# Performance work log

Hardware: AMD Instinct MI355X
Metric: run time of the kernel (lower is better)

The kernel has to match this reference:

```python
import jax, jax.numpy as jnp
import numpy as np

NUM_CLASSES = 80
STRIDES = (32, 16, 8)
SCORE_THRESH = 0.01
NMS_THRESH = 0.45
TOP_K = 200
PRE_K = 4096          # pre-NMS candidate cap (greedy NMS only ever emits TOP_K boxes)
NEG = -1e9            # 'suppressed' score sentinel (avoids -inf NaN issues)
CLS_OFFSET = 4096.0   # class-aware NMS: offset boxes per class (boxes live in [0, 608])

_ANCHORS_PX = [[(116, 90), (156, 198), (373, 326)],
               [(30, 61), (62, 45), (59, 119)],
               [(10, 13), (16, 30), (33, 23)]]


def setup_inputs() -> dict:
    key = jax.random.key(0)
    bs, img = 8, 608
    inp = {}
    for lvl, (stride, anc) in enumerate(zip(STRIDES, _ANCHORS_PX)):
        H = W = img // stride
        key, k = jax.random.split(key)
        inp[f"in{lvl}"] = jax.random.normal(k, (bs, 3 * (NUM_CLASSES + 5), H, W), dtype=jnp.float32)
        aw = jnp.array([a[0] / stride for a in anc], jnp.float32)
        ah = jnp.array([a[1] / stride for a in anc], jnp.float32)
        inp[f"aw{lvl}"] = jnp.broadcast_to(aw[None, :, None, None], (bs, 3, H, W))
        inp[f"ah{lvl}"] = jnp.broadcast_to(ah[None, :, None, None], (bs, 3, H, W))
        inp[f"gx{lvl}"] = jnp.broadcast_to(jnp.arange(W, dtype=jnp.float32)[None, None, None, :], (bs, 3, H, W))
        inp[f"gy{lvl}"] = jnp.broadcast_to(jnp.arange(H, dtype=jnp.float32)[None, None, :, None], (bs, 3, H, W))
    return inp


def _decode_level(x, aw, ah, gx, gy, stride):
    bs, _, H, W = x.shape
    x = x.reshape(bs, -1, NUM_CLASSES + 5, H, W).transpose(0, 1, 3, 4, 2)  # [bs,3,H,W,85]
    px = jax.nn.sigmoid(x[..., 0]) + gx
    py = jax.nn.sigmoid(x[..., 1]) + gy
    pw = jnp.exp(x[..., 2]) * aw
    ph = jnp.exp(x[..., 3]) * ah
    conf = jax.nn.sigmoid(x[..., 4])
    cls = jax.nn.sigmoid(x[..., 5:])
    boxes = jnp.stack([px, py, pw, ph], -1) * jnp.float32(stride)  # [bs,3,H,W,4] (cx,cy,w,h)
    return boxes.reshape(bs, -1, 4), conf.reshape(bs, -1), cls.reshape(bs, -1, NUM_CLASSES)


def _center_to_corner(b):
    cx, cy, w, h = b[..., 0], b[..., 1], b[..., 2], b[..., 3]
    return jnp.stack([cx - w / 2, cy - h / 2, cx + w / 2, cy + h / 2], -1)


def _nms_image(boxes, conf, cls):
    # boxes [N,4] corner, conf [N], cls [N,C]
    N, C = cls.shape
    scores = (conf[:, None] * cls).reshape(-1)                          # [N*C]
    cboxes = jnp.broadcast_to(boxes[:, None, :], (N, C, 4)).reshape(-1, 4)
    labels = jnp.broadcast_to(jnp.arange(C), (N, C)).reshape(-1)
    s = jnp.where(scores > SCORE_THRESH, scores, NEG)
    top_s, idx = jax.lax.top_k(s, PRE_K)
    b = cboxes[idx]                                                     # [PRE_K,4]
    l = labels[idx]
    ob = b + (l.astype(jnp.float32) * CLS_OFFSET)[:, None]              # class-aware offset
    area = (ob[:, 2] - ob[:, 0]) * (ob[:, 3] - ob[:, 1])

    def step(live, _):
        i = jnp.argmax(live)
        si, bi, ai = live[i], ob[i], area[i]
        x1 = jnp.maximum(bi[0], ob[:, 0]); y1 = jnp.maximum(bi[1], ob[:, 1])
        x2 = jnp.minimum(bi[2], ob[:, 2]); y2 = jnp.minimum(bi[3], ob[:, 3])
        inter = jnp.clip(x2 - x1, 0.0) * jnp.clip(y2 - y1, 0.0)
        iou = inter / (ai + area - inter + 1e-9)
        live = jnp.where(iou > NMS_THRESH, NEG, live)                   # suppresses self too
        return live, (i, si)

    _, (sel, sel_s) = jax.lax.scan(step, top_s, None, length=TOP_K)
    valid = sel_s > SCORE_THRESH
    out_b = jnp.where(valid[:, None], b[sel], 0.0)
    out_l = jnp.where(valid, l[sel], 0).astype(jnp.float32)
    out_s = jnp.where(valid, sel_s, 0.0)
    return jnp.concatenate([out_b, out_l[:, None], out_s[:, None]], -1)  # [TOP_K, 6]


def _forward(levels):
    boxes, conf, cls = [], [], []
    for (x, aw, ah, gx, gy), stride in zip(levels, STRIDES):
        bb, cc, cl = _decode_level(x, aw, ah, gx, gy, stride)
        boxes.append(bb); conf.append(cc); cls.append(cl)
    boxes = _center_to_corner(jnp.concatenate(boxes, 1))   # [bs,N,4]
    conf = jnp.concatenate(conf, 1)                        # [bs,N]
    cls = jnp.concatenate(cls, 1)                          # [bs,N,C]
    return jax.vmap(_nms_image)(boxes, conf, cls)          # [bs,TOP_K,6]


def reference(in0, aw0, ah0, gx0, gy0, in1, aw1, ah1, gx1, gy1, in2, aw2, ah2, gx2, gy2):
    levels = [(in0, aw0, ah0, gx0, gy0), (in1, aw1, ah1, gx1, gy1), (in2, aw2, ah2, gx2, gy2)]
    return _forward(levels)
```

## Files before the change

### kernel.cpp

```cpp
#include <hip/hip_runtime.h>
#include <stdint.h>

typedef unsigned int u32;
typedef unsigned long long u64;

#define NCLS 80
#define NBOX 22743
#define PREK 4096
#define BCAP 65536
#define NIMG 8
#define SCORE_TH 0.01f
#define IOU_TH 0.45f
#define TOPK 200

#define DCH 20
#define DNCH 4
#define GCH 10
#define GNCH 8

#define LCAP 1536

#define BKCAP 8
#define HCAP 224
#define HUGE_TH 3488.0f

#define RJC 4
#define RJW 1024

#define CBINS 512
#define CBIN_BASE 7680u

#define HIST_OFF 0
#define CNT_OFF  16384
#define ZERO_BYTES 18432
#define WIN_OFF  18432
#define BND_OFF  280576
#define PART_OFF BND_OFF
#define BOX_OFF  4474880
#define SKEY_OFF 7385984
#define SOBOX_OFF 7648128
#define SAREA_OFF 8172416

__device__ __forceinline__ float sigmf(float x) { return 1.0f / (1.0f + expf(-x)); }

__device__ __forceinline__ u64 pad_key(int i) { return (u64)(~(u32)i); }

__global__ __launch_bounds__(256) void init_k(uint4* __restrict__ ws) {
  const int i = blockIdx.x * 256 + threadIdx.x;
  if (i < ZERO_BYTES / 16) ws[i] = make_uint4(0u, 0u, 0u, 0u);
}

__global__ __launch_bounds__(256) void decode_hist_all(const float* __restrict__ in0,
                              const float* __restrict__ in1, const float* __restrict__ in2,
                              float4* __restrict__ boxes, u32* __restrict__ hist) {
  __shared__ u32 lh[CBINS];
  const int img = blockIdx.y;
  const int c0 = blockIdx.z * DCH;
  for (int i = threadIdx.x; i < CBINS; i += 256) lh[i] = 0;
  __syncthreads();

  const int bx = blockIdx.x;
  if (bx < 5) {
    const int W = 19, HW = 361;
    const int r = bx * 256 + threadIdx.x;
    if (r < 3 * HW) {
      const int a = r / HW, p = r - a * HW;
      const int y = p / W, x = p - y * W;
      const float* base = in0 + ((size_t)(img * 255 + a * 85)) * (size_t)HW + p;
      float l[DCH];
#pragma unroll
      for (int k = 0; k < DCH; ++k) l[k] = base[(size_t)(5 + c0 + k) * HW];
      const float x4 = base[4 * (size_t)HW];
      if (c0 == 0) {
        const float aw = (a == 0) ? 3.625f : ((a == 1) ? 4.875f : 11.65625f);
        const float ah = (a == 0) ? 2.8125f : ((a == 1) ? 6.1875f : 10.1875f);
        const float x0 = base[0];
        const float x1 = base[(size_t)HW];
        const float x2 = base[2 * (size_t)HW];
        const float x3 = base[3 * (size_t)HW];
        const float px = sigmf(x0) + (float)x;
        const float py = sigmf(x1) + (float)y;
        const float pw = expf(x2) * aw;
        const float ph = expf(x3) * ah;
        const float cx = px * 32.f, cy = py * 32.f, bw = pw * 32.f, bh = ph * 32.f;
        boxes[(size_t)img * NBOX + r] =
            make_float4(cx - bw * 0.5f, cy - bh * 0.5f, cx + bw * 0.5f, cy + bh * 0.5f);
      }
      const float conf = sigmf(x4);
      if (conf > SCORE_TH) {
#pragma unroll
        for (int k = 0; k < DCH; ++k) {
          float s = conf * sigmf(l[k]);
          if (s > SCORE_TH) {
            u32 bin = (__float_as_uint(s) >> 17) - CBIN_BASE;
            atomicAdd(&lh[bin], 1u);
          }
        }
      }
    }
  } else {
    const bool L1 = bx < 10;
    const float* in = L1 ? in1 : in2;
    const int W = L1 ? 38 : 76;
    const int HW = L1 ? 1444 : 5776;
    const int lvl_off = L1 ? 1083 : 5415;
    const float stride = L1 ? 16.f : 8.f;
    const int HW4 = HW >> 2;
    const int idx = (bx - (L1 ? 5 : 10)) * 256 + threadIdx.x;
    if (idx < 3 * HW4) {
      const int a = idx / HW4;
      const int p0 = (idx - a * HW4) << 2;
      const float* base = in + ((size_t)(img * 255 + a * 85)) * (size_t)HW + p0;
      float4 scv[DCH];
#pragma unroll
      for (int k = 0; k < DCH; ++k)
        scv[k] = *(const float4*)(base + (size_t)(5 + c0 + k) * HW);
      float4 v4 = *(const float4*)(base + 4 * (size_t)HW);
      const float* t4 = (const float*)&v4;
      float conf[4];
      if (c0 == 0) {
        const float aw = L1 ? ((a == 0) ? 1.875f : ((a == 1) ? 3.875f : 3.6875f))
                            : ((a == 0) ? 1.25f : ((a == 1) ? 2.f : 4.125f));
        const float ah = L1 ? ((a == 0) ? 3.8125f : ((a == 1) ? 2.8125f : 7.4375f))
                            : ((a == 0) ? 1.625f : ((a == 1) ? 3.75f : 2.875f));
        float4 v0 = *(const float4*)(base);
        float4 v1 = *(const float4*)(base + (size_t)HW);
        float4 v2 = *(const float4*)(base + 2 * (size_t)HW);
        float4 v3 = *(const float4*)(base + 3 * (size_t)HW);
        const float* t0 = (const float*)&v0;
        const float* t1 = (const float*)&v1;
        const float* t2 = (const float*)&v2;
        const float* t3 = (const float*)&v3;
        float4* bout = boxes + (size_t)img * NBOX + lvl_off + a * HW + p0;
#pragma unroll
        for (int i = 0; i < 4; ++i) {
          const int p = p0 + i;
          const int y = p / W, x = p - y * W;
          const float px = sigmf(t0[i]) + (float)x;
          const float py = sigmf(t1[i]) + (float)y;
          const float pw = expf(t2[i]) * aw;
          const float ph = expf(t3[i]) * ah;
          const float cx = px * stride, cy = py * stride, bw = pw * stride, bh = ph * stride;
          bout[i] = make_float4(cx - bw * 0.5f, cy - bh * 0.5f, cx + bw * 0.5f, cy + bh * 0.5f);
        }
      }
#pragma unroll
      for (int i = 0; i < 4; ++i) conf[i] = sigmf(t4[i]);
#pragma unroll
      for (int k = 0; k < DCH; ++k) {
        const float* s4 = (const float*)&scv[k];
#pragma unroll
        for (int i = 0; i < 4; ++i) {
          float s = conf[i] * sigmf(s4[i]);
          if (s > SCORE_TH) {
            u32 bin = (__float_as_uint(s) >> 17) - CBIN_BASE;
            atomicAdd(&lh[bin], 1u);
          }
        }
      }
    }
  }
  __syncthreads();
  u32* gh = hist + (size_t)img * CBINS;
  for (int i = threadIdx.x; i < CBINS; i += 256) {
    u32 v = lh[i];
    if (v) atomicAdd(&gh[i], v);
  }
}

__device__ __forceinline__ void flush_list(const u64* llist, int lcnt, int cap,
                                           int* gctr, u64* glist, int gcap) {
  __shared__ int gbase_s;
  int n = lcnt < cap ? lcnt : cap;
  if (threadIdx.x == 0) gbase_s = n ? atomicAdd(gctr, n) : 0;
  __syncthreads();
  const int gb = gbase_s;
  for (int i = threadIdx.x; i < n; i += 256) {
    int pos = gb + i;
    if (pos < gcap) glist[pos] = llist[i];
  }
}

__global__ __launch_bounds__(256) void gather_all(const float* __restrict__ in0,
                         const float* __restrict__ in1, const float* __restrict__ in2,
                         const u32* __restrict__ hist, int* __restrict__ cnt,
                         u64* __restrict__ winners, u64* __restrict__ boundary) {
  __shared__ u64 lwin[LCAP];
  __shared__ u64 lbnd[LCAP];
  __shared__ int lwc, lbc;
  __shared__ u32 s_wsum[4];
  __shared__ int sB;
  const int img = blockIdx.y;
  const int c0 = blockIdx.z * GCH;
  const int t = threadIdx.x;
  if (t == 0) { lwc = 0; lbc = 0; sB = -1; }

  {
    const u32* gh = hist + (size_t)img * CBINS;
    u32 hv0 = gh[t * 2], hv1 = gh[t * 2 + 1];
    u32 s = hv0 + hv1;
    const int lane = t & 63;
    u32 v = s;
#pragma unroll
    for (int off = 1; off < 64; off <<= 1) {
      u32 o = __shfl_down(v, off);
      if (lane + off < 64) v += o;
    }
    if (lane == 0) s_wsum[t >> 6] = v;
    __syncthreads();
    u32 hi = 0;
    for (int w = (t >> 6) + 1; w < 4; ++w) hi += s_wsum[w];
    const u32 above = hi + (v - s);
    if (above < (u32)PREK && above + s >= (u32)PREK) {
      u32 cum = above + hv1;
      if (cum >= (u32)PREK) sB = t * 2 + 1;
      else sB = t * 2;
    }
    __syncthreads();
  }
  const int B = sB;

  int* cw = &cnt[img * 64];
  int* cb = &cnt[img * 64 + 32];
  u64* wl = winners + (size_t)img * PREK;
  u64* bl = boundary + (size_t)img * BCAP;
  const int bx = blockIdx.x;

  if (bx < 5) {
    const int HW = 361;
    const int r = bx * 256 + t;
    if (r < 3 * HW) {
      const int a = r / HW, p = r - a * HW;
      const float* base = in0 + ((size_t)(img * 255 + a * 85)) * (size_t)HW + p;
      const int boxg = r;
      float l[GCH];
#pragma unroll
      for (int k = 0; k < GCH; ++k) l[k] = base[(size_t)(5 + c0 + k) * HW];
      const float conf = sigmf(base[4 * (size_t)HW]);
#pragma unroll
      for (int k = 0; k < GCH; ++k) {
        float s = conf * sigmf(l[k]);
        if (s > SCORE_TH) {
          u32 key = __float_as_uint(s);
          int wbin = (int)((key >> 17) - CBIN_BASE);
          if (wbin >= B) {
            u64 kv = ((u64)key << 32) | (u64)(~(u32)(boxg * NCLS + (c0 + k)));
            if (wbin > B) {
              int p2 = atomicAdd(&lwc, 1);
              if (p2 < LCAP) lwin[p2] = kv;
              else { int g = atomicAdd(cw, 1); if (g < PREK) wl[g] = kv; }
            } else {
              int p2 = atomicAdd(&lbc, 1);
              if (p2 < LCAP) lbnd[p2] = kv;
              else { int g = atomicAdd(cb, 1); if (g < BCAP) bl[g] = kv; }
            }
          }
        }
      }
    }
  } else {
    const bool L1 = bx < 10;
    const float* in = L1 ? in1 : in2;
    const int HW = L1 ? 1444 : 5776;
    const int lvl_off = L1 ? 1083 : 5415;
    const int HW4 = HW >> 2;
    const int idx = (bx - (L1 ? 5 : 10)) * 256 + t;
    if (idx < 3 * HW4) {
      const int a = idx / HW4;
      const int p0 = (idx - a * HW4) << 2;
      const float* base = in + ((size_t)(img * 255 + a * 85)) * (size_t)HW + p0;
      const int boxg0 = lvl_off + a * HW + p0;
      float4 scv[GCH];
#pragma unroll
      for (int k = 0; k < GCH; ++k)
        scv[k] = *(const float4*)(base + (size_t)(5 + c0 + k) * HW);
      float4 v4 = *(const float4*)(base + 4 * (size_t)HW);
      const float* t4 = (const float*)&v4;
      float conf[4];
#pragma unroll
      for (int i = 0; i < 4; ++i) conf[i] = sigmf(t4[i]);
#pragma unroll
      for (int k = 0; k < GCH; ++k) {
        const float* s4 = (const float*)&scv[k];
        const int c = c0 + k;
#pragma unroll
        for (int i = 0; i < 4; ++i) {
          float s = conf[i] * sigmf(s4[i]);
          if (s > SCORE_TH) {
            u32 key = __float_as_uint(s);
            int wbin = (int)((key >> 17) - CBIN_BASE);
            if (wbin >= B) {
              u64 kv = ((u64)key << 32) | (u64)(~(u32)((boxg0 + i) * NCLS + c));
              if (wbin > B) {
                int p = atomicAdd(&lwc, 1);
                if (p < LCAP) lwin[p] = kv;
                else { int g = atomicAdd(cw, 1); if (g < PREK) wl[g] = kv; }
              } else {
                int p = atomicAdd(&lbc, 1);
                if (p < LCAP) lbnd[p] = kv;
                else { int g = atomicAdd(cb, 1); if (g < BCAP) bl[g] = kv; }
              }
            }
          }
        }
      }
    }
  }
  __syncthreads();
  flush_list(lwin, lwc, LCAP, cw, wl, PREK);
  flush_list(lbnd, lbc, LCAP, cb, bl, BCAP);
}

__global__ void resolve_k(const u64* __restrict__ boundary,
                          int* __restrict__ cnt, u64* __restrict__ winners) {
  const int img = blockIdx.x;
  const int cw_pre = cnt[img * 64];
  const int T = PREK - cw_pre;
  int bc = cnt[img * 64 + 32];
  if (bc > BCAP) bc = BCAP;
  if (T <= 0 || bc <= 0) return;
  const u64* bnd = boundary + (size_t)img * BCAP;
  u64* wl = winners + (size_t)img * PREK;
  int* cw = &cnt[img * 64];

  __shared__ u32 h2[16384];
  __shared__ u32 lsum[256];
  __shared__ u32 above[256];
  __shared__ u32 s_total;
  __shared__ int sB2, sT2;
  __shared__ u64 ties[512];
  __shared__ int tcnt;
  __shared__ u64 lw2[PREK];
  __shared__ int lw2c;
  __shared__ int gbase_s;
  const int t = threadIdx.x;
  for (int i = t; i < 16384; i += 256) h2[i] = 0;
  if (t == 0) { tcnt = 0; sB2 = -1; sT2 = 0; lw2c = 0; }
  __syncthreads();
  for (int i = t; i < bc; i += 256) atomicAdd(&h2[(u32)(bnd[i] >> 35) & 0x3FFFu], 1u);
  __syncthreads();
  u32 s = 0;
  for (int j = 0; j < 64; ++j) s += h2[t * 64 + j];
  lsum[t] = s;
  __syncthreads();
  if (t == 0) {
    u32 acc = 0;
    for (int i = 255; i >= 0; --i) { above[i] = acc; acc += lsum[i]; }
    s_total = acc;
  }
  __syncthreads();
  if ((int)s_total > T) {
    if (above[t] < (u32)T && above[t] + lsum[t] >= (u32)T) {
      u32 cum = above[t];
      for (int j = 63; j >= 0; --j) {
        u32 hv = h2[t * 64 + j];
        cum += hv;
        if (cum >= (u32)T) { sB2 = t * 64 + j; sT2 = (int)((u32)T - (cum - hv)); break; }
      }
    }
  }
  __syncthreads();
  const int B2 = sB2, T2 = sT2;
  for (int i = t; i < bc; i += 256) {
    u64 e = bnd[i];
    int low = (int)((u32)(e >> 35) & 0x3FFFu);
    if (low > B2) {
      int p = atomicAdd(&lw2c, 1);
      if (p < PREK) lw2[p] = e;
    } else if (low == B2) {
      int tp = atomicAdd(&tcnt, 1);
      if (tp < 512) ties[tp] = e;
    }
  }
  __syncthreads();
  int n = lw2c < PREK ? lw2c : PREK;
  if (t == 0) gbase_s = n ? atomicAdd(cw, n) : 0;
  __syncthreads();
  for (int i = t; i < n; i += 256) {
    int pos = gbase_s + i;
    if (pos < PREK) wl[pos] = lw2[i];
  }
  __syncthreads();
  if (t == 0 && T2 > 0) {
    int tc = tcnt < 512 ? tcnt : 512;
    for (int k = 0; k < T2 && k < tc; ++k) {
      int bi = -1; u64 bk = 0;
      for (int i = 0; i < tc; ++i)
        if (ties[i] > bk) { bk = ties[i]; bi = i; }
      if (bi < 0) break;
      ties[bi] = 0;
      int pos = atomicAdd(cw, 1);
      if (pos < PREK) wl[pos] = bk;
    }
  }
}

__global__ __launch_bounds__(256) void rank_part_k(const u64* __restrict__ winners,
                                                   const int* __restrict__ cnt,
                                                   int* __restrict__ part) {
  __shared__ u64 lk[RJW];
  const int img = blockIdx.y;
  const int kc = blockIdx.x >> 2;
  const int jc = blockIdx.x & 3;
  const int t = threadIdx.x;
  int wc = cnt[img * 64]; if (wc > PREK) wc = PREK;
  const u64* wl = winners + (size_t)img * PREK;
  for (int i = t; i < RJW; i += 256) {
    const int gj = jc * RJW + i;
    lk[i] = (gj < wc) ? wl[gj] : pad_key(gj);
  }
  __syncthreads();
  const int ki_idx = kc * 256 + t;
  const u64 ki = (ki_idx < wc) ? wl[ki_idx] : pad_key(ki_idx);
  int rank = 0;
#pragma unroll 8
  for (int j = 0; j < RJW; ++j) rank += (lk[j] > ki) ? 1 : 0;
  part[(((size_t)img * RJC) + jc) * PREK + ki_idx] = rank;
}

__global__ __launch_bounds__(256) void rank_scatter_k(const u64* __restrict__ winners,
                                              const int* __restrict__ cnt,
                                              const int* __restrict__ part,
                                              const float4* __restrict__ boxes,
                                              u64* __restrict__ skey,
                                              float4* __restrict__ sobox,
                                              float* __restrict__ sarea) {
  const int img = blockIdx.y;
  const int i = blockIdx.x * 256 + threadIdx.x;
  int wc = cnt[img * 64]; if (wc > PREK) wc = PREK;
  const u64* wl = winners + (size_t)img * PREK;
  const u64 ki = (i < wc) ? wl[i] : pad_key(i);
  const int* pb = part + (size_t)img * RJC * PREK + i;
  int rank = pb[0] + pb[PREK] + pb[2 * PREK] + pb[3 * PREK];
  skey[(size_t)img * PREK + rank] = ki;
  if (i < wc) {
    u32 ridx = ~(u32)ki;
    int c = (int)(ridx % NCLS);
    int bi = (int)(ridx / NCLS);
    float4 b = boxes[(size_t)img * NBOX + bi];
    float off = 4096.0f * (float)c;
    float4 ob = make_float4(b.x + off, b.y + off, b.z + off, b.w + off);
    sobox[(size_t)img * PREK + rank] = ob;
    sarea[(size_t)img * PREK + rank] = (ob.z - ob.x) * (ob.w - ob.y);
  } else {
    sobox[(size_t)img * PREK + rank] = make_float4(0.f, 0.f, 0.f, 0.f);
    sarea[(size_t)img * PREK + rank] = 0.f;
  }
}

__global__ __launch_bounds__(64) void scan_nms_k(const u64* __restrict__ skey,
                                                 const float4* __restrict__ sobox,
                                                 const float* __restrict__ sarea,
                                                 float* __restrict__ out) {
  __shared__ float4 bxc[NCLS][BKCAP];
  __shared__ float  arc[NCLS][BKCAP];
  __shared__ int    cntc[NCLS];
  __shared__ float4 bxa[TOPK];
  __shared__ float  ara[TOPK];
  __shared__ float4 bxh[HCAP];
  __shared__ float  arh[HCAP];
  __shared__ int    nhuge_s;
  __shared__ float4 chb[64];
  __shared__ float  cha[64];
  const int img = blockIdx.x;
  const int lane = threadIdx.x;
  float* orow = out + (size_t)img * (TOPK * 6);
  for (int i = lane; i < TOPK * 6; i += 64) orow[i] = 0.f;
  for (int i = lane; i < NCLS; i += 64) cntc[i] = 0;
  if (lane == 0) nhuge_s = 0;
  const u64* K = skey + (size_t)img * PREK;
  const float4* Bp = sobox + (size_t)img * PREK;
  const float* Ap = sarea + (size_t)img * PREK;
  int nsel = 0;
  u64 kj = K[lane];
  float4 ob = Bp[lane];
  float ar = Ap[lane];
  for (int chunk = 0; chunk < PREK / 64 && nsel < TOPK; ++chunk) {
    u64 kj_n = 0ull; float4 ob_n = make_float4(0.f, 0.f, 0.f, 0.f); float ar_n = 0.f;
    if (chunk + 1 < PREK / 64) {
      const int jn = (chunk + 1) * 64 + lane;
      kj_n = K[jn]; ob_n = Bp[jn]; ar_n = Ap[jn];
    }
    const float score = __uint_as_float((u32)(kj >> 32));
    bool alive = (score > SCORE_TH);
    if (__ballot(alive) == 0ull) break;
    const u32 ridx = ~(u32)kj;
    const int myc = (int)(ridx % NCLS);
    const bool huge = (ob.z - ob.x > HUGE_TH) || (ob.w - ob.y > HUGE_TH);
    chb[lane] = ob; cha[lane] = ar;

    u64 mm = ~0ull;
#pragma unroll
    for (int k = 0; k < 7; ++k) {
      const u64 bk = __ballot(((myc >> k) & 1) != 0);
      mm &= (((myc >> k) & 1) != 0) ? bk : ~bk;
    }
    const u64 hb = __ballot(huge);

    {
      const int n0 = cntc[myc];
      const int n = n0 < BKCAP ? n0 : BKCAP;
      for (int k = 0; k < n && alive; ++k) {
        const float4 b0 = bxc[myc][k]; const float a0 = arc[myc][k];
        float xx1 = fmaxf(b0.x, ob.x), yy1 = fmaxf(b0.y, ob.y);
        float xx2 = fminf(b0.z, ob.z), yy2 = fminf(b0.w, ob.w);
        float inter = fmaxf(xx2 - xx1, 0.f) * fmaxf(yy2 - yy1, 0.f);
        float iou = inter / (a0 + ar - inter + 1e-9f);
        if (iou > IOU_TH) alive = false;
      }
    }
    {
      const int nh = nhuge_s;
      for (int k = 0; k < nh; ++k) {
        if (alive) {
          const float4 b0 = bxh[k]; const float a0 = arh[k];
          float xx1 = fmaxf(b0.x, ob.x), yy1 = fmaxf(b0.y, ob.y);
          float xx2 = fminf(b0.z, ob.z), yy2 = fminf(b0.w, ob.w);
          float inter = fmaxf(xx2 - xx1, 0.f) * fmaxf(yy2 - yy1, 0.f);
          float iou = inter / (a0 + ar - inter + 1e-9f);
          if (iou > IOU_TH) alive = false;
        }
      }
    }
    if (__ballot(alive && huge) != 0ull) {
      const int na = nsel;
      for (int k = 0; k < na; ++k) {
        if (alive && huge) {
          const float4 b0 = bxa[k]; const float a0 = ara[k];
          float xx1 = fmaxf(b0.x, ob.x), yy1 = fmaxf(b0.y, ob.y);
          float xx2 = fminf(b0.z, ob.z), yy2 = fminf(b0.w, ob.w);
          float inter = fmaxf(xx2 - xx1, 0.f) * fmaxf(yy2 - yy1, 0.f);
          float iou = inter / (a0 + ar - inter + 1e-9f);
          if (iou > IOU_TH) alive = false;
        }
      }
    }
    const u64 amask = __ballot(alive);
    const u64 below = (1ull << lane) - 1ull;
    u64 tm = alive ? ((mm | hb | (huge ? ~0ull : 0ull)) & below & amask) : 0ull;
    u64 sup = 0ull;
    while (tm) {
      const int tb = (int)__builtin_ctzll(tm);
      tm &= tm - 1ull;
      const float4 bj = chb[tb];
      const float aj = cha[tb];
      float xx1 = fmaxf(bj.x, ob.x), yy1 = fmaxf(bj.y, ob.y);
      float xx2 = fminf(bj.z, ob.z), yy2 = fminf(bj.w, ob.w);
      float inter = fmaxf(xx2 - xx1, 0.f) * fmaxf(yy2 - yy1, 0.f);
      float iou = inter / (aj + ar - inter + 1e-9f);
      if (iou > IOU_TH) sup |= (1ull << tb);
    }
    u64 rem = amask;
    u64 selbits = 0ull;
    while (rem != 0ull && nsel + (int)__popcll(selbits) < TOPK) {
      const int b = __builtin_ctzll(rem);
      selbits |= (1ull << b);
      rem &= ~(1ull << b);
      const u64 colb = __ballot((sup >> b) & 1ull);
      rem &= ~colb;
    }
    const bool selme = (selbits >> lane) & 1ull;
    if (selme) {
      const int slot = nsel + (int)__popcll(selbits & ((1ull << lane) - 1ull));
      bxa[slot] = ob; ara[slot] = ar;
      if (!huge) {
        int cc = atomicAdd(&cntc[myc], 1);
        if (cc < BKCAP) { bxc[myc][cc] = ob; arc[myc][cc] = ar; }
        else { int hn = atomicAdd(&nhuge_s, 1); if (hn < HCAP) { bxh[hn] = ob; arh[hn] = ar; } }
      } else {
        int hn = atomicAdd(&nhuge_s, 1);
        if (hn < HCAP) { bxh[hn] = ob; arh[hn] = ar; }
      }
      const float off = 4096.0f * (float)myc;
      orow[slot * 6 + 0] = ob.x - off;
      orow[slot * 6 + 1] = ob.y - off;
      orow[slot * 6 + 2] = ob.z - off;
      orow[slot * 6 + 3] = ob.w - off;
      orow[slot * 6 + 4] = (float)myc;
      orow[slot * 6 + 5] = score;
    }
    nsel += (int)__popcll(selbits);
    kj = kj_n; ob = ob_n; ar = ar_n;
  }
}

extern "C" void kernel_launch(void* const* d_in, const int* in_sizes, int n_in,
                              void* d_out, int out_size, void* d_ws, size_t ws_size,
                              hipStream_t stream) {
  const float* in0 = (const float*)d_in[0];
  const float* in1 = (const float*)d_in[5];
  const float* in2 = (const float*)d_in[10];
  char* ws = (char*)d_ws;
  u32* hist = (u32*)(ws + HIST_OFF);
  int* cnt = (int*)(ws + CNT_OFF);
  u64* winners = (u64*)(ws + WIN_OFF);
  u64* boundary = (u64*)(ws + BND_OFF);
  int* part = (int*)(ws + PART_OFF);
  float4* boxes = (float4*)(ws + BOX_OFF);
  u64* skey = (u64*)(ws + SKEY_OFF);
  float4* sobox = (float4*)(ws + SOBOX_OFF);
  float* sarea = (float*)(ws + SAREA_OFF);
  float* out = (float*)d_out;

  init_k<<<(ZERO_BYTES / 16 + 255) / 256, 256, 0, stream>>>((uint4*)ws);

  decode_hist_all<<<dim3(27, 8, DNCH), 256, 0, stream>>>(in0, in1, in2, boxes, hist);

  gather_all<<<dim3(27, 8, GNCH), 256, 0, stream>>>(in0, in1, in2, hist, cnt, winners, boundary);

  resolve_k<<<8, 256, 0, stream>>>(boundary, cnt, winners);

  rank_part_k<<<dim3(64, 8), 256, 0, stream>>>(winners, cnt, part);
  rank_scatter_k<<<dim3(16, 8), 256, 0, stream>>>(winners, cnt, part, boxes, skey, sobox, sarea);
  scan_nms_k<<<8, 64, 0, stream>>>(skey, sobox, sarea, out);
}
```

Baseline: 113.2 us.

## Record per-anchor max score bin in decode to skip gather reloads

The decode/histogram pass now writes, per anchor and class chunk, the highest histogram bin reached as a 16-bit value. The gather pass reads this value first and skips loading the class logits whenever that bin is below the threshold bin, so most anchors no longer re-read their logits. Gather also switches to the decode pass's 20-class chunking (4 z-slices instead of 8), and the boundary buffer cap is halved to make room in the workspace. The cost is an extra small write and read per anchor, plus a risk of overflow if the boundary list ever exceeds the smaller cap.

```diff
diff --git a/kernel.cpp b/kernel.cpp
--- a/kernel.cpp
+++ b/kernel.cpp
@@ -2,12 +2,13 @@
 #include <stdint.h>
 
 typedef unsigned int u32;
+typedef unsigned short u16;
 typedef unsigned long long u64;
 
 #define NCLS 80
 #define NBOX 22743
 #define PREK 4096
-#define BCAP 65536
+#define BCAP 32768
 #define NIMG 8
 #define SCORE_TH 0.01f
 #define IOU_TH 0.45f
@@ -15,8 +16,6 @@
 
 #define DCH 20
 #define DNCH 4
-#define GCH 10
-#define GNCH 8
 
 #define LCAP 1536
 
@@ -29,6 +28,10 @@
 
 #define CBINS 512
 #define CBIN_BASE 7680u
+
+#define PMSTRIDE 22752
+#define PML1 1088
+#define PML2 5424
 
 #define HIST_OFF 0
 #define CNT_OFF  16384
@@ -36,10 +39,11 @@
 #define WIN_OFF  18432
 #define BND_OFF  280576
 #define PART_OFF BND_OFF
-#define BOX_OFF  4474880
-#define SKEY_OFF 7385984
-#define SOBOX_OFF 7648128
-#define SAREA_OFF 8172416
+#define PMAX_OFF 2377728
+#define BOX_OFF  3833856
+#define SKEY_OFF 6744960
+#define SOBOX_OFF 7007104
+#define SAREA_OFF 7531392
 
 __device__ __forceinline__ float sigmf(float x) { return 1.0f / (1.0f + expf(-x)); }
 
@@ -52,12 +56,15 @@
 
 __global__ __launch_bounds__(256) void decode_hist_all(const float* __restrict__ in0,
                               const float* __restrict__ in1, const float* __restrict__ in2,
-                              float4* __restrict__ boxes, u32* __restrict__ hist) {
+                              float4* __restrict__ boxes, u32* __restrict__ hist,
+                              u16* __restrict__ pmax) {
   __shared__ u32 lh[CBINS];
   const int img = blockIdx.y;
-  const int c0 = blockIdx.z * DCH;
+  const int cz = blockIdx.z;
+  const int c0 = cz * DCH;
   for (int i = threadIdx.x; i < CBINS; i += 256) lh[i] = 0;
   __syncthreads();
+  u16* pmc = pmax + ((size_t)(img * DNCH + cz)) * PMSTRIDE;
 
   const int bx = blockIdx.x;
   if (bx < 5) {
@@ -87,16 +94,19 @@
             make_float4(cx - bw * 0.5f, cy - bh * 0.5f, cx + bw * 0.5f, cy + bh * 0.5f);
       }
       const float conf = sigmf(x4);
+      u32 pm = 0;
       if (conf > SCORE_TH) {
 #pragma unroll
         for (int k = 0; k < DCH; ++k) {
           float s = conf * sigmf(l[k]);
           if (s > SCORE_TH) {
             u32 bin = (__float_as_uint(s) >> 17) - CBIN_BASE;
+            pm = pm > bin ? pm : bin;
             atomicAdd(&lh[bin], 1u);
           }
         }
       }
+      pmc[r] = (u16)pm;
     }
   } else {
     const bool L1 = bx < 10;
@@ -104,6 +114,7 @@
     const int W = L1 ? 38 : 76;
     const int HW = L1 ? 1444 : 5776;
     const int lvl_off = L1 ? 1083 : 5415;
+    const int pm_off = L1 ? PML1 : PML2;
     const float stride = L1 ? 16.f : 8.f;
     const int HW4 = HW >> 2;
     const int idx = (bx - (L1 ? 5 : 10)) * 256 + threadIdx.x;
@@ -146,6 +157,7 @@
       }
 #pragma unroll
       for (int i = 0; i < 4; ++i) conf[i] = sigmf(t4[i]);
+      u32 pmb[4] = {0u, 0u, 0u, 0u};
 #pragma unroll
       for (int k = 0; k < DCH; ++k) {
         const float* s4 = (const float*)&scv[k];
@@ -154,10 +166,13 @@
           float s = conf[i] * sigmf(s4[i]);
           if (s > SCORE_TH) {
             u32 bin = (__float_as_uint(s) >> 17) - CBIN_BASE;
+            pmb[i] = pmb[i] > bin ? pmb[i] : bin;
             atomicAdd(&lh[bin], 1u);
           }
         }
       }
+      const u64 pk = (u64)pmb[0] | ((u64)pmb[1] << 16) | ((u64)pmb[2] << 32) | ((u64)pmb[3] << 48);
+      *(u64*)(pmc + pm_off + a * HW + p0) = pk;
     }
   }
   __syncthreads();
@@ -183,7 +198,8 @@
 
 __global__ __launch_bounds__(256) void gather_all(const float* __restrict__ in0,
                          const float* __restrict__ in1, const float* __restrict__ in2,
-                         const u32* __restrict__ hist, int* __restrict__ cnt,
+                         const u32* __restrict__ hist, const u16* __restrict__ pmax,
+                         int* __restrict__ cnt,
                          u64* __restrict__ winners, u64* __restrict__ boundary) {
   __shared__ u64 lwin[LCAP];
   __shared__ u64 lbnd[LCAP];
@@ -191,7 +207,8 @@
   __shared__ u32 s_wsum[4];
   __shared__ int sB;
   const int img = blockIdx.y;
-  const int c0 = blockIdx.z * GCH;
+  const int cz = blockIdx.z;
+  const int c0 = cz * DCH;
   const int t = threadIdx.x;
   if (t == 0) { lwc = 0; lbc = 0; sB = -1; }
 
@@ -220,6 +237,7 @@
   }
   const int B = sB;
 
+  const u16* pmc = pmax + ((size_t)(img * DNCH + cz)) * PMSTRIDE;
   int* cw = &cnt[img * 64];
   int* cb = &cnt[img * 64 + 32];
   u64* wl = winners + (size_t)img * PREK;
@@ -229,16 +247,16 @@
   if (bx < 5) {
     const int HW = 361;
     const int r = bx * 256 + t;
-    if (r < 3 * HW) {
+    if (r < 3 * HW && (int)pmc[r] >= B) {
       const int a = r / HW, p = r - a * HW;
       const float* base = in0 + ((size_t)(img * 255 + a * 85)) * (size_t)HW + p;
       const int boxg = r;
-      float l[GCH];
-#pragma unroll
-      for (int k = 0; k < GCH; ++k) l[k] = base[(size_t)(5 + c0 + k) * HW];
+      float l[DCH];
+#pragma unroll
+      for (int k = 0; k < DCH; ++k) l[k] = base[(size_t)(5 + c0 + k) * HW];
       const float conf = sigmf(base[4 * (size_t)HW]);
 #pragma unroll
-      for (int k = 0; k < GCH; ++k) {
+      for (int k = 0; k < DCH; ++k) {
         float s = conf * sigmf(l[k]);
         if (s > SCORE_TH) {
           u32 key = __float_as_uint(s);
@@ -263,42 +281,49 @@
     const float* in = L1 ? in1 : in2;
     const int HW = L1 ? 1444 : 5776;
     const int lvl_off = L1 ? 1083 : 5415;
+    const int pm_off = L1 ? PML1 : PML2;
     const int HW4 = HW >> 2;
     const int idx = (bx - (L1 ? 5 : 10)) * 256 + t;
     if (idx < 3 * HW4) {
       const int a = idx / HW4;
       const int p0 = (idx - a * HW4) << 2;
-      const float* base = in + ((size_t)(img * 255 + a * 85)) * (size_t)HW + p0;
-      const int boxg0 = lvl_off + a * HW + p0;
-      float4 scv[GCH];
-#pragma unroll
-      for (int k = 0; k < GCH; ++k)
-        scv[k] = *(const float4*)(base + (size_t)(5 + c0 + k) * HW);
-      float4 v4 = *(const float4*)(base + 4 * (size_t)HW);
-      const float* t4 = (const float*)&v4;
-      float conf[4];
-#pragma unroll
-      for (int i = 0; i < 4; ++i) conf[i] = sigmf(t4[i]);
-#pragma unroll
-      for (int k = 0; k < GCH; ++k) {
-        const float* s4 = (const float*)&scv[k];
-        const int c = c0 + k;
-#pragma unroll
-        for (int i = 0; i < 4; ++i) {
-          float s = conf[i] * sigmf(s4[i]);
-          if (s > SCORE_TH) {
-            u32 key = __float_as_uint(s);
-            int wbin = (int)((key >> 17) - CBIN_BASE);
-            if (wbin >= B) {
-              u64 kv = ((u64)key << 32) | (u64)(~(u32)((boxg0 + i) * NCLS + c));
-              if (wbin > B) {
-                int p = atomicAdd(&lwc, 1);
-                if (p < LCAP) lwin[p] = kv;
-                else { int g = atomicAdd(cw, 1); if (g < PREK) wl[g] = kv; }
-              } else {
-                int p = atomicAdd(&lbc, 1);
-                if (p < LCAP) lbnd[p] = kv;
-                else { int g = atomicAdd(cb, 1); if (g < BCAP) bl[g] = kv; }
+      const u64 pk = *(const u64*)(pmc + pm_off + a * HW + p0);
+      const int m0 = (int)(pk & 0xFFFF), m1 = (int)((pk >> 16) & 0xFFFF);
+      const int m2 = (int)((pk >> 32) & 0xFFFF), m3 = (int)((pk >> 48) & 0xFFFF);
+      int mx = m0 > m1 ? m0 : m1; mx = mx > m2 ? mx : m2; mx = mx > m3 ? mx : m3;
+      if (mx >= B) {
+        const float* base = in + ((size_t)(img * 255 + a * 85)) * (size_t)HW + p0;
+        const int boxg0 = lvl_off + a * HW + p0;
+        float4 scv[DCH];
+#pragma unroll
+        for (int k = 0; k < DCH; ++k)
+          scv[k] = *(const float4*)(base + (size_t)(5 + c0 + k) * HW);
+        float4 v4 = *(const float4*)(base + 4 * (size_t)HW);
+        const float* t4 = (const float*)&v4;
+        float conf[4];
+#pragma unroll
+        for (int i = 0; i < 4; ++i) conf[i] = sigmf(t4[i]);
+#pragma unroll
+        for (int k = 0; k < DCH; ++k) {
+          const float* s4 = (const float*)&scv[k];
+          const int c = c0 + k;
+#pragma unroll
+          for (int i = 0; i < 4; ++i) {
+            float s = conf[i] * sigmf(s4[i]);
+            if (s > SCORE_TH) {
+              u32 key = __float_as_uint(s);
+              int wbin = (int)((key >> 17) - CBIN_BASE);
+              if (wbin >= B) {
+                u64 kv = ((u64)key << 32) | (u64)(~(u32)((boxg0 + i) * NCLS + c));
+                if (wbin > B) {
+                  int p = atomicAdd(&lwc, 1);
+                  if (p < LCAP) lwin[p] = kv;
+                  else { int g = atomicAdd(cw, 1); if (g < PREK) wl[g] = kv; }
+                } else {
+                  int p = atomicAdd(&lbc, 1);
+                  if (p < LCAP) lbnd[p] = kv;
+                  else { int g = atomicAdd(cb, 1); if (g < BCAP) bl[g] = kv; }
+                }
               }
             }
           }
@@ -596,6 +621,7 @@
   u64* winners = (u64*)(ws + WIN_OFF);
   u64* boundary = (u64*)(ws + BND_OFF);
   int* part = (int*)(ws + PART_OFF);
+  u16* pmax = (u16*)(ws + PMAX_OFF);
   float4* boxes = (float4*)(ws + BOX_OFF);
   u64* skey = (u64*)(ws + SKEY_OFF);
   float4* sobox = (float4*)(ws + SOBOX_OFF);
@@ -604,9 +630,9 @@
 
   init_k<<<(ZERO_BYTES / 16 + 255) / 256, 256, 0, stream>>>((uint4*)ws);
 
-  decode_hist_all<<<dim3(27, 8, DNCH), 256, 0, stream>>>(in0, in1, in2, boxes, hist);
-
-  gather_all<<<dim3(27, 8, GNCH), 256, 0, stream>>>(in0, in1, in2, hist, cnt, winners, boundary);
+  decode_hist_all<<<dim3(27, 8, DNCH), 256, 0, stream>>>(in0, in1, in2, boxes, hist, pmax);
+
+  gather_all<<<dim3(27, 8, DNCH), 256, 0, stream>>>(in0, in1, in2, hist, pmax, cnt, winners, boundary);
 
   resolve_k<<<8, 256, 0, stream>>>(boundary, cnt, winners);
 
```

After: 119.6 us. 1.06x slower.
